# Kernel tuning notes

Measured on AMD Instinct MI355X. Metric: run time of the kernel, lower is better.

The kernel has to match this reference:

```python
import jax, jax.numpy as jnp
import numpy as np

N_NODES = 50000
TAU = 1.0 + (1.0 / 1000.0) * (0.1 - 1.0)  # anneal step 1 -> 0.9991


def setup_inputs() -> dict:
    key = jax.random.key(0)
    ks = jax.random.split(key, 8)
    N, F, H, E, K = N_NODES, 128, 128, 800000, 5
    node_features = jax.random.normal(ks[0], (N, F), dtype=jnp.float32)
    src = jnp.sort(jax.random.randint(ks[1], (E,), 0, N, dtype=jnp.int32))
    dst = jax.random.randint(ks[2], (E,), 0, N, dtype=jnp.int32)
    u_noise = jax.random.uniform(ks[3], (K, E), dtype=jnp.float32,
                                 minval=1e-6, maxval=1.0 - 1e-6)
    # MLP params: Linear(2F -> H), ReLU, Linear(H -> 1)
    W1 = jax.random.normal(ks[4], (2 * F, H), dtype=jnp.float32) / np.sqrt(2 * F)
    b1 = jnp.zeros((H,), dtype=jnp.float32)
    W2 = jax.random.normal(ks[5], (H, 1), dtype=jnp.float32) / np.sqrt(H)
    b2 = jnp.zeros((1,), dtype=jnp.float32)
    return {"node_features": node_features, "W1": W1, "b1": b1,
            "W2": W2, "b2": b2, "u_noise": u_noise, "src": src, "dst": dst}


def reference(node_features, W1, b1, W2, b2, u_noise, src, dst):
    N = N_NODES
    F = node_features.shape[1]
    # per-edge MLP on concat([x_u, x_v]) without materializing the (E, 2F) concat
    x_u = node_features[src]                      # (E, F)
    x_v = node_features[dst]                      # (E, F)
    h = jax.nn.relu(x_u @ W1[:F] + x_v @ W1[F:] + b1)   # (E, H)
    z = (h @ W2 + b2)[:, 0]                       # (E,)
    # per-node (segment) log-softmax over each node's neighbor edges
    zmax = jax.ops.segment_max(z, src, num_segments=N)
    ze = z - zmax[src]
    denom = jax.ops.segment_sum(jnp.exp(ze), src, num_segments=N)
    log_pi = ze - jnp.log(denom)[src]             # (E,)
    # k rounds of Gumbel-softmax sampling
    g = -jnp.log(-jnp.log(u_noise))               # (K, E)
    scores = (log_pi[None, :] + g) / TAU          # (K, E)

    def seg_softmax(s):
        m = jax.ops.segment_max(s, src, num_segments=N)
        e = jnp.exp(s - m[src])
        return e / jax.ops.segment_sum(e, src, num_segments=N)[src]

    def seg_argmax_dst(s):
        m = jax.ops.segment_max(s, src, num_segments=N)
        hit = s >= m[src]
        sel = jax.ops.segment_max(jnp.where(hit, dst, -1), src, num_segments=N)
        return sel  # (N,) selected neighbor per node, per round

    soft = jax.vmap(seg_softmax)(scores)          # (K, E) gumbel-softmax probs
    selected = jax.vmap(seg_argmax_dst)(scores)   # (K, N) sampled neighbor ids
    return selected, soft
```

## Files before the change

### kernel.cpp

```cpp
#include <hip/hip_runtime.h>

#define FEAT 128
#define HID  128
#define XS_S 132

__global__ __launch_bounds__(256) void gemm_ab(
    const float* __restrict__ X, const float* __restrict__ W1,
    float* __restrict__ A, float* __restrict__ B, int N) {
  __shared__ float xs[32 * XS_S];
  __shared__ float ws[32 * 64];
  const int t = threadIdx.x;
  const int n0 = blockIdx.x * 128;
  const int j0 = blockIdx.y * 64;
  const float* Wbase = W1 + (j0 < 128 ? j0 : 128 * HID + (j0 - 128));
  float* Obase = (j0 < 128) ? (A + j0) : (B + (j0 - 128));

  const int tn = t & 31;
  const int tc = t >> 5;

  float acc[4][8];
#pragma unroll
  for (int r = 0; r < 4; ++r)
#pragma unroll
    for (int c = 0; c < 8; ++c) acc[r][c] = 0.f;

  const int ln = t >> 3;
  const int lf = (t & 7) * 4;

  for (int kc = 0; kc < 4; ++kc) {
    __syncthreads();
#pragma unroll
    for (int rep = 0; rep < 4; ++rep) {
      const int nl = ln + rep * 32;
      const int n = n0 + nl;
      float4 v = make_float4(0.f, 0.f, 0.f, 0.f);
      if (n < N) v = *(const float4*)(X + (size_t)n * FEAT + kc * 32 + lf);
      xs[(lf + 0) * XS_S + nl] = v.x;
      xs[(lf + 1) * XS_S + nl] = v.y;
      xs[(lf + 2) * XS_S + nl] = v.z;
      xs[(lf + 3) * XS_S + nl] = v.w;
    }
#pragma unroll
    for (int rep = 0; rep < 2; ++rep) {
      const int idx = rep * 256 + t;
      const int r = idx >> 4;
      const int c4 = (idx & 15) * 4;
      *(float4*)&ws[r * 64 + c4] =
          *(const float4*)(Wbase + (size_t)(kc * 32 + r) * HID + c4);
    }
    __syncthreads();

#pragma unroll 8
    for (int k = 0; k < 32; ++k) {
      const float4 xv = *(const float4*)&xs[k * XS_S + tn * 4];
      const float4 w0 = *(const float4*)&ws[k * 64 + tc * 8];
      const float4 w1 = *(const float4*)&ws[k * 64 + tc * 8 + 4];
      const float xr[4] = {xv.x, xv.y, xv.z, xv.w};
#pragma unroll
      for (int r = 0; r < 4; ++r) {
        acc[r][0] = fmaf(xr[r], w0.x, acc[r][0]);
        acc[r][1] = fmaf(xr[r], w0.y, acc[r][1]);
        acc[r][2] = fmaf(xr[r], w0.z, acc[r][2]);
        acc[r][3] = fmaf(xr[r], w0.w, acc[r][3]);
        acc[r][4] = fmaf(xr[r], w1.x, acc[r][4]);
        acc[r][5] = fmaf(xr[r], w1.y, acc[r][5]);
        acc[r][6] = fmaf(xr[r], w1.z, acc[r][6]);
        acc[r][7] = fmaf(xr[r], w1.w, acc[r][7]);
      }
    }
  }

#pragma unroll
  for (int r = 0; r < 4; ++r) {
    const int n = n0 + tn * 4 + r;
    if (n < N) {
      float* o = Obase + (size_t)n * HID + tc * 8;
      *(float4*)o = make_float4(acc[r][0], acc[r][1], acc[r][2], acc[r][3]);
      *(float4*)(o + 4) = make_float4(acc[r][4], acc[r][5], acc[r][6], acc[r][7]);
    }
  }
}

__global__ __launch_bounds__(256) void row_offsets(
    const int* __restrict__ src, int* __restrict__ rs, int N, int E) {
  const int n = blockIdx.x * 256 + threadIdx.x;
  if (n > N) return;
  int lo = 0, hi = E;
  while (lo < hi) {
    const int mid = (lo + hi) >> 1;
    if (src[mid] < n) lo = mid + 1; else hi = mid;
  }
  rs[n] = lo;
}

__global__ __launch_bounds__(256) void edge_z(
    const float* __restrict__ A, const float* __restrict__ B,
    const float* __restrict__ b1, const float* __restrict__ W2,
    const float* __restrict__ b2, const int* __restrict__ src,
    const int* __restrict__ dst, float* __restrict__ z, int E) {
  const int g = threadIdx.x >> 4;
  const int l = threadIdx.x & 15;
  const int e0 = blockIdx.x * 32 + g * 2;
  if (e0 >= E) return;
  const int e1 = e0 + 1;
  const bool has1 = e1 < E;

  const int u0 = src[e0], v0 = dst[e0];
  const int u1 = has1 ? src[e1] : u0;
  const int v1 = has1 ? dst[e1] : v0;

  const float4* Au0 = (const float4*)(A + (size_t)u0 * HID) + l * 2;
  const float4* Bv0 = (const float4*)(B + (size_t)v0 * HID) + l * 2;
  const float4* Au1 = (const float4*)(A + (size_t)u1 * HID) + l * 2;
  const float4* Bv1 = (const float4*)(B + (size_t)v1 * HID) + l * 2;

  const float4 a00 = Au0[0], a01 = Au0[1];
  const float4 b00 = Bv0[0], b01 = Bv0[1];
  const float4 a10 = Au1[0], a11 = Au1[1];
  const float4 b10 = Bv1[0], b11 = Bv1[1];

  const float4 c0 = *(const float4*)(b1 + l * 8);
  const float4 c1 = *(const float4*)(b1 + l * 8 + 4);
  const float4 w0 = *(const float4*)(W2 + l * 8);
  const float4 w1 = *(const float4*)(W2 + l * 8 + 4);
  const float bias2 = b2[0];

  float p0 = fmaxf(a00.x + b00.x + c0.x, 0.f) * w0.x
           + fmaxf(a00.y + b00.y + c0.y, 0.f) * w0.y
           + fmaxf(a00.z + b00.z + c0.z, 0.f) * w0.z
           + fmaxf(a00.w + b00.w + c0.w, 0.f) * w0.w
           + fmaxf(a01.x + b01.x + c1.x, 0.f) * w1.x
           + fmaxf(a01.y + b01.y + c1.y, 0.f) * w1.y
           + fmaxf(a01.z + b01.z + c1.z, 0.f) * w1.z
           + fmaxf(a01.w + b01.w + c1.w, 0.f) * w1.w;
  float p1 = fmaxf(a10.x + b10.x + c0.x, 0.f) * w0.x
           + fmaxf(a10.y + b10.y + c0.y, 0.f) * w0.y
           + fmaxf(a10.z + b10.z + c0.z, 0.f) * w0.z
           + fmaxf(a10.w + b10.w + c0.w, 0.f) * w0.w
           + fmaxf(a11.x + b11.x + c1.x, 0.f) * w1.x
           + fmaxf(a11.y + b11.y + c1.y, 0.f) * w1.y
           + fmaxf(a11.z + b11.z + c1.z, 0.f) * w1.z
           + fmaxf(a11.w + b11.w + c1.w, 0.f) * w1.w;

#pragma unroll
  for (int m = 8; m >= 1; m >>= 1) {
    p0 += __shfl_xor(p0, m);
    p1 += __shfl_xor(p1, m);
  }
  if (l == 0) {
    z[e0] = p0 + bias2;
    if (has1) z[e1] = p1 + bias2;
  }
}

__global__ __launch_bounds__(256) void seg_sample(
    const float* __restrict__ z, const float* __restrict__ U,
    const int* __restrict__ dst, const int* __restrict__ rs,
    float* __restrict__ out_sel, float* __restrict__ out_soft,
    int N, int E, int K) {
  const int t = threadIdx.x;
  const int lane = t & 63;
  const int half = lane >> 5;
  const int hl = lane & 31;
  const int n = blockIdx.x * 8 + (t >> 6) * 2 + half;
  const float INVTAU = 1.0f / 0.9991f;

  int start = 0, deg = 0;
  if (n < N) { start = rs[n]; deg = rs[n + 1] - start; }

  if (__all(deg <= 32)) {
    if (n >= N) return;
    if (deg == 0) {
      if (hl == 0)
        for (int k = 0; k < K; ++k) out_sel[(size_t)k * N + n] = -2147483648.0f;
      return;
    }
    const bool act = hl < deg;
    const int e = start + (act ? hl : 0);
    const float zv = act ? z[e] : -INFINITY;
    const int d = act ? dst[e] : -1;

    float zmax = zv;
#pragma unroll
    for (int m = 16; m >= 1; m >>= 1) zmax = fmaxf(zmax, __shfl_xor(zmax, m));
    float den = act ? __expf(zv - zmax) : 0.f;
#pragma unroll
    for (int m = 16; m >= 1; m >>= 1) den += __shfl_xor(den, m);
    const float lpb = (zv - zmax) - __logf(den);

    for (int k = 0; k < K; ++k) {
      float ex = 0.f;
      if (act) {
        const float uu = U[(size_t)k * E + e];
        const float t2 = -__logf(uu);
        const float g = -__logf(t2);
        ex = __expf((lpb + g) * INVTAU);
      }
      float d2 = ex;
      float mx = ex;
      int md = d;
#pragma unroll
      for (int m = 16; m >= 1; m >>= 1) {
        d2 += __shfl_xor(d2, m);
        const float ox = __shfl_xor(mx, m);
        const int od = __shfl_xor(md, m);
        if (ox > mx) { mx = ox; md = od; }
        else if (ox == mx) md = max(md, od);
      }
      if (hl == 0) out_sel[(size_t)k * N + n] = (float)md;
      if (act) {
        const float inv = __builtin_amdgcn_rcpf(d2);
        out_soft[(size_t)k * E + e] = ex * inv;
      }
    }
    return;
  }

  const int wbase = blockIdx.x * 8 + (t >> 6) * 2;
  for (int j = 0; j < 2; ++j) {
    const int nn = wbase + j;
    if (nn >= N) continue;
    const int st = rs[nn];
    const int dg = rs[nn + 1] - st;
    if (dg == 0) {
      if (lane == 0)
        for (int k = 0; k < K; ++k) out_sel[(size_t)k * N + nn] = -2147483648.0f;
      continue;
    }
    float zmax = -INFINITY;
    for (int c = lane; c < dg; c += 64) zmax = fmaxf(zmax, z[st + c]);
#pragma unroll
    for (int m = 32; m >= 1; m >>= 1) zmax = fmaxf(zmax, __shfl_xor(zmax, m));
    float den = 0.f;
    for (int c = lane; c < dg; c += 64) den += expf(z[st + c] - zmax);
#pragma unroll
    for (int m = 32; m >= 1; m >>= 1) den += __shfl_xor(den, m);
    const float logd = logf(den);

    for (int k = 0; k < K; ++k) {
      float m2 = -INFINITY;
      for (int c = lane; c < dg; c += 64) {
        const int e = st + c;
        const float g = -logf(-logf(U[(size_t)k * E + e]));
        const float s = ((z[e] - zmax) - logd + g) * INVTAU;
        m2 = fmaxf(m2, s);
      }
#pragma unroll
      for (int m = 32; m >= 1; m >>= 1) m2 = fmaxf(m2, __shfl_xor(m2, m));
      float d2 = 0.f;
      int cand = -1;
      for (int c = lane; c < dg; c += 64) {
        const int e = st + c;
        const float g = -logf(-logf(U[(size_t)k * E + e]));
        const float s = ((z[e] - zmax) - logd + g) * INVTAU;
        d2 += expf(s - m2);
        if (s >= m2) cand = max(cand, dst[e]);
      }
#pragma unroll
      for (int m = 32; m >= 1; m >>= 1) d2 += __shfl_xor(d2, m);
#pragma unroll
      for (int m = 32; m >= 1; m >>= 1) cand = max(cand, __shfl_xor(cand, m));
      if (lane == 0) out_sel[(size_t)k * N + nn] = (float)cand;
      for (int c = lane; c < dg; c += 64) {
        const int e = st + c;
        const float g = -logf(-logf(U[(size_t)k * E + e]));
        const float s = ((z[e] - zmax) - logd + g) * INVTAU;
        out_soft[(size_t)k * E + e] = expf(s - m2) / d2;
      }
    }
  }
}

extern "C" void kernel_launch(void* const* d_in, const int* in_sizes, int n_in,
                              void* d_out, int out_size, void* d_ws, size_t ws_size,
                              hipStream_t stream) {
  const float* X  = (const float*)d_in[0];
  const float* W1 = (const float*)d_in[1];
  const float* b1 = (const float*)d_in[2];
  const float* W2 = (const float*)d_in[3];
  const float* b2 = (const float*)d_in[4];
  const float* U  = (const float*)d_in[5];
  const int* src  = (const int*)d_in[6];
  const int* dst  = (const int*)d_in[7];
  const int E = in_sizes[6];
  const int K = in_sizes[5] / E;
  const int N = in_sizes[0] / FEAT;

  float* A = (float*)d_ws;
  float* B = A + (size_t)N * HID;
  float* z = B + (size_t)N * HID;
  int* rs  = (int*)(z + E);

  float* out_sel  = (float*)d_out;
  float* out_soft = (float*)d_out + (size_t)K * N;

  hipLaunchKernelGGL(gemm_ab, dim3((N + 127) / 128, 4), dim3(256), 0, stream,
                     X, W1, A, B, N);
  hipLaunchKernelGGL(row_offsets, dim3((N + 256) / 256), dim3(256), 0, stream,
                     src, rs, N, E);
  hipLaunchKernelGGL(edge_z, dim3((E + 31) / 32), dim3(256), 0, stream,
                     A, B, b1, W2, b2, src, dst, z, E);
  hipLaunchKernelGGL(seg_sample, dim3((N + 7) / 8), dim3(256), 0, stream,
                     z, U, dst, rs, out_sel, out_soft, N, E, K);
}
```

Measured before the change: 241.4 us.

## Widen GEMM tile with XCD-aware block mapping, fold b1, 16-lane segment sampling

The node GEMM now computes all 128 output columns per block, so each thread holds a 4x16 accumulator instead of 4x8 and the X tile is loaded half as often. A 1D grid is remapped so neighbouring node tiles land on the same XCD. The b1 bias is added once per node in the GEMM epilogue rather than per edge in edge_z. seg_sample now assigns 16 lanes per node, each handling two edges, which cuts shuffle steps and packs more nodes per wave but makes the __all(deg<=32) fast path slower for high-degree nodes and raises GEMM register pressure.

```diff
diff --git a/kernel.cpp b/kernel.cpp
--- a/kernel.cpp
+++ b/kernel.cpp
@@ -6,23 +6,29 @@
 
 __global__ __launch_bounds__(256) void gemm_ab(
     const float* __restrict__ X, const float* __restrict__ W1,
-    float* __restrict__ A, float* __restrict__ B, int N) {
+    const float* __restrict__ b1, float* __restrict__ A,
+    float* __restrict__ B, int N) {
   __shared__ float xs[32 * XS_S];
-  __shared__ float ws[32 * 64];
+  __shared__ float ws[32 * 128];
   const int t = threadIdx.x;
-  const int n0 = blockIdx.x * 128;
-  const int j0 = blockIdx.y * 64;
-  const float* Wbase = W1 + (j0 < 128 ? j0 : 128 * HID + (j0 - 128));
-  float* Obase = (j0 < 128) ? (A + j0) : (B + (j0 - 128));
+
+  const int nb = gridDim.x;
+  const int q = nb >> 3, r = nb & 7;
+  const int xcd = blockIdx.x & 7, bidx = blockIdx.x >> 3;
+  const int nw = (xcd < r ? xcd * (q + 1) : r * (q + 1) + (xcd - r) * q) + bidx;
+  const int n0 = (nw >> 1) * 128;
+  const int g = nw & 1;
+  const float* Wbase = W1 + (size_t)g * 128 * HID;
+  float* Obase = g ? B : A;
 
   const int tn = t & 31;
   const int tc = t >> 5;
 
-  float acc[4][8];
-#pragma unroll
-  for (int r = 0; r < 4; ++r)
-#pragma unroll
-    for (int c = 0; c < 8; ++c) acc[r][c] = 0.f;
+  float acc[4][16];
+#pragma unroll
+  for (int rr = 0; rr < 4; ++rr)
+#pragma unroll
+    for (int c = 0; c < 16; ++c) acc[rr][c] = 0.f;
 
   const int ln = t >> 3;
   const int lf = (t & 7) * 4;
@@ -41,42 +47,63 @@
       xs[(lf + 3) * XS_S + nl] = v.w;
     }
 #pragma unroll
-    for (int rep = 0; rep < 2; ++rep) {
+    for (int rep = 0; rep < 4; ++rep) {
       const int idx = rep * 256 + t;
-      const int r = idx >> 4;
-      const int c4 = (idx & 15) * 4;
-      *(float4*)&ws[r * 64 + c4] =
-          *(const float4*)(Wbase + (size_t)(kc * 32 + r) * HID + c4);
+      const int wr = idx >> 5;
+      const int c4 = (idx & 31) * 4;
+      *(float4*)&ws[wr * 128 + c4] =
+          *(const float4*)(Wbase + (size_t)(kc * 32 + wr) * HID + c4);
     }
     __syncthreads();
 
 #pragma unroll 8
     for (int k = 0; k < 32; ++k) {
       const float4 xv = *(const float4*)&xs[k * XS_S + tn * 4];
-      const float4 w0 = *(const float4*)&ws[k * 64 + tc * 8];
-      const float4 w1 = *(const float4*)&ws[k * 64 + tc * 8 + 4];
+      const float4 w0 = *(const float4*)&ws[k * 128 + tc * 16 + 0];
+      const float4 w1 = *(const float4*)&ws[k * 128 + tc * 16 + 4];
+      const float4 w2 = *(const float4*)&ws[k * 128 + tc * 16 + 8];
+      const float4 w3 = *(const float4*)&ws[k * 128 + tc * 16 + 12];
       const float xr[4] = {xv.x, xv.y, xv.z, xv.w};
 #pragma unroll
-      for (int r = 0; r < 4; ++r) {
-        acc[r][0] = fmaf(xr[r], w0.x, acc[r][0]);
-        acc[r][1] = fmaf(xr[r], w0.y, acc[r][1]);
-        acc[r][2] = fmaf(xr[r], w0.z, acc[r][2]);
-        acc[r][3] = fmaf(xr[r], w0.w, acc[r][3]);
-        acc[r][4] = fmaf(xr[r], w1.x, acc[r][4]);
-        acc[r][5] = fmaf(xr[r], w1.y, acc[r][5]);
-        acc[r][6] = fmaf(xr[r], w1.z, acc[r][6]);
-        acc[r][7] = fmaf(xr[r], w1.w, acc[r][7]);
-      }
-    }
-  }
-
-#pragma unroll
-  for (int r = 0; r < 4; ++r) {
-    const int n = n0 + tn * 4 + r;
+      for (int rr = 0; rr < 4; ++rr) {
+        acc[rr][0]  = fmaf(xr[rr], w0.x, acc[rr][0]);
+        acc[rr][1]  = fmaf(xr[rr], w0.y, acc[rr][1]);
+        acc[rr][2]  = fmaf(xr[rr], w0.z, acc[rr][2]);
+        acc[rr][3]  = fmaf(xr[rr], w0.w, acc[rr][3]);
+        acc[rr][4]  = fmaf(xr[rr], w1.x, acc[rr][4]);
+        acc[rr][5]  = fmaf(xr[rr], w1.y, acc[rr][5]);
+        acc[rr][6]  = fmaf(xr[rr], w1.z, acc[rr][6]);
+        acc[rr][7]  = fmaf(xr[rr], w1.w, acc[rr][7]);
+        acc[rr][8]  = fmaf(xr[rr], w2.x, acc[rr][8]);
+        acc[rr][9]  = fmaf(xr[rr], w2.y, acc[rr][9]);
+        acc[rr][10] = fmaf(xr[rr], w2.z, acc[rr][10]);
+        acc[rr][11] = fmaf(xr[rr], w2.w, acc[rr][11]);
+        acc[rr][12] = fmaf(xr[rr], w3.x, acc[rr][12]);
+        acc[rr][13] = fmaf(xr[rr], w3.y, acc[rr][13]);
+        acc[rr][14] = fmaf(xr[rr], w3.z, acc[rr][14]);
+        acc[rr][15] = fmaf(xr[rr], w3.w, acc[rr][15]);
+      }
+    }
+  }
+
+  float4 bb[4];
+#pragma unroll
+  for (int c = 0; c < 4; ++c) bb[c] = make_float4(0.f, 0.f, 0.f, 0.f);
+  if (g == 0) {
+#pragma unroll
+    for (int c = 0; c < 4; ++c) bb[c] = *(const float4*)(b1 + tc * 16 + c * 4);
+  }
+#pragma unroll
+  for (int rr = 0; rr < 4; ++rr) {
+    const int n = n0 + tn * 4 + rr;
     if (n < N) {
-      float* o = Obase + (size_t)n * HID + tc * 8;
-      *(float4*)o = make_float4(acc[r][0], acc[r][1], acc[r][2], acc[r][3]);
-      *(float4*)(o + 4) = make_float4(acc[r][4], acc[r][5], acc[r][6], acc[r][7]);
+      float* o = Obase + (size_t)n * HID + tc * 16;
+#pragma unroll
+      for (int c = 0; c < 4; ++c) {
+        *(float4*)(o + c * 4) = make_float4(
+            acc[rr][c * 4 + 0] + bb[c].x, acc[rr][c * 4 + 1] + bb[c].y,
+            acc[rr][c * 4 + 2] + bb[c].z, acc[rr][c * 4 + 3] + bb[c].w);
+      }
     }
   }
 }
@@ -95,9 +122,9 @@
 
 __global__ __launch_bounds__(256) void edge_z(
     const float* __restrict__ A, const float* __restrict__ B,
-    const float* __restrict__ b1, const float* __restrict__ W2,
-    const float* __restrict__ b2, const int* __restrict__ src,
-    const int* __restrict__ dst, float* __restrict__ z, int E) {
+    const float* __restrict__ W2, const float* __restrict__ b2,
+    const int* __restrict__ src, const int* __restrict__ dst,
+    float* __restrict__ z, int E) {
   const int g = threadIdx.x >> 4;
   const int l = threadIdx.x & 15;
   const int e0 = blockIdx.x * 32 + g * 2;
@@ -119,28 +146,26 @@
   const float4 a10 = Au1[0], a11 = Au1[1];
   const float4 b10 = Bv1[0], b11 = Bv1[1];
 
-  const float4 c0 = *(const float4*)(b1 + l * 8);
-  const float4 c1 = *(const float4*)(b1 + l * 8 + 4);
   const float4 w0 = *(const float4*)(W2 + l * 8);
   const float4 w1 = *(const float4*)(W2 + l * 8 + 4);
   const float bias2 = b2[0];
 
-  float p0 = fmaxf(a00.x + b00.x + c0.x, 0.f) * w0.x
-           + fmaxf(a00.y + b00.y + c0.y, 0.f) * w0.y
-           + fmaxf(a00.z + b00.z + c0.z, 0.f) * w0.z
-           + fmaxf(a00.w + b00.w + c0.w, 0.f) * w0.w
-           + fmaxf(a01.x + b01.x + c1.x, 0.f) * w1.x
-           + fmaxf(a01.y + b01.y + c1.y, 0.f) * w1.y
-           + fmaxf(a01.z + b01.z + c1.z, 0.f) * w1.z
-           + fmaxf(a01.w + b01.w + c1.w, 0.f) * w1.w;
-  float p1 = fmaxf(a10.x + b10.x + c0.x, 0.f) * w0.x
-           + fmaxf(a10.y + b10.y + c0.y, 0.f) * w0.y
-           + fmaxf(a10.z + b10.z + c0.z, 0.f) * w0.z
-           + fmaxf(a10.w + b10.w + c0.w, 0.f) * w0.w
-           + fmaxf(a11.x + b11.x + c1.x, 0.f) * w1.x
-           + fmaxf(a11.y + b11.y + c1.y, 0.f) * w1.y
-           + fmaxf(a11.z + b11.z + c1.z, 0.f) * w1.z
-           + fmaxf(a11.w + b11.w + c1.w, 0.f) * w1.w;
+  float p0 = fmaxf(a00.x + b00.x, 0.f) * w0.x
+           + fmaxf(a00.y + b00.y, 0.f) * w0.y
+           + fmaxf(a00.z + b00.z, 0.f) * w0.z
+           + fmaxf(a00.w + b00.w, 0.f) * w0.w
+           + fmaxf(a01.x + b01.x, 0.f) * w1.x
+           + fmaxf(a01.y + b01.y, 0.f) * w1.y
+           + fmaxf(a01.z + b01.z, 0.f) * w1.z
+           + fmaxf(a01.w + b01.w, 0.f) * w1.w;
+  float p1 = fmaxf(a10.x + b10.x, 0.f) * w0.x
+           + fmaxf(a10.y + b10.y, 0.f) * w0.y
+           + fmaxf(a10.z + b10.z, 0.f) * w0.z
+           + fmaxf(a10.w + b10.w, 0.f) * w0.w
+           + fmaxf(a11.x + b11.x, 0.f) * w1.x
+           + fmaxf(a11.y + b11.y, 0.f) * w1.y
+           + fmaxf(a11.z + b11.z, 0.f) * w1.z
+           + fmaxf(a11.w + b11.w, 0.f) * w1.w;
 
 #pragma unroll
   for (int m = 8; m >= 1; m >>= 1) {
@@ -160,9 +185,9 @@
     int N, int E, int K) {
   const int t = threadIdx.x;
   const int lane = t & 63;
-  const int half = lane >> 5;
-  const int hl = lane & 31;
-  const int n = blockIdx.x * 8 + (t >> 6) * 2 + half;
+  const int qtr = lane >> 4;
+  const int ql = lane & 15;
+  const int n = blockIdx.x * 16 + (t >> 6) * 4 + qtr;
   const float INVTAU = 1.0f / 0.9991f;
 
   int start = 0, deg = 0;
@@ -171,53 +196,65 @@
   if (__all(deg <= 32)) {
     if (n >= N) return;
     if (deg == 0) {
-      if (hl == 0)
+      if (ql == 0)
         for (int k = 0; k < K; ++k) out_sel[(size_t)k * N + n] = -2147483648.0f;
       return;
     }
-    const bool act = hl < deg;
-    const int e = start + (act ? hl : 0);
-    const float zv = act ? z[e] : -INFINITY;
-    const int d = act ? dst[e] : -1;
-
-    float zmax = zv;
-#pragma unroll
-    for (int m = 16; m >= 1; m >>= 1) zmax = fmaxf(zmax, __shfl_xor(zmax, m));
-    float den = act ? __expf(zv - zmax) : 0.f;
-#pragma unroll
-    for (int m = 16; m >= 1; m >>= 1) den += __shfl_xor(den, m);
-    const float lpb = (zv - zmax) - __logf(den);
+    const bool a0 = 2 * ql < deg;
+    const bool a1 = 2 * ql + 1 < deg;
+    const int e0 = start + 2 * ql;
+    const int e1 = e0 + 1;
+    const float z0 = a0 ? z[e0] : -INFINITY;
+    const float z1 = a1 ? z[e1] : -INFINITY;
+    const int d0 = a0 ? dst[e0] : -1;
+    const int d1 = a1 ? dst[e1] : -1;
+
+    float zmax = fmaxf(z0, z1);
+#pragma unroll
+    for (int m = 8; m >= 1; m >>= 1) zmax = fmaxf(zmax, __shfl_xor(zmax, m));
+    float den = (a0 ? __expf(z0 - zmax) : 0.f) + (a1 ? __expf(z1 - zmax) : 0.f);
+#pragma unroll
+    for (int m = 8; m >= 1; m >>= 1) den += __shfl_xor(den, m);
+    const float logd = __logf(den);
+    const float lp0 = (z0 - zmax) - logd;
+    const float lp1 = (z1 - zmax) - logd;
 
     for (int k = 0; k < K; ++k) {
-      float ex = 0.f;
-      if (act) {
-        const float uu = U[(size_t)k * E + e];
-        const float t2 = -__logf(uu);
-        const float g = -__logf(t2);
-        ex = __expf((lpb + g) * INVTAU);
-      }
-      float d2 = ex;
-      float mx = ex;
-      int md = d;
-#pragma unroll
-      for (int m = 16; m >= 1; m >>= 1) {
+      float ex0 = 0.f, ex1 = 0.f;
+      if (a0) {
+        const float uu = U[(size_t)k * E + e0];
+        const float gum = -__logf(-__logf(uu));
+        ex0 = __expf((lp0 + gum) * INVTAU);
+      }
+      if (a1) {
+        const float uu = U[(size_t)k * E + e1];
+        const float gum = -__logf(-__logf(uu));
+        ex1 = __expf((lp1 + gum) * INVTAU);
+      }
+      float d2 = ex0 + ex1;
+      float mx;
+      int md;
+      if (ex1 > ex0)      { mx = ex1; md = d1; }
+      else if (ex1 < ex0) { mx = ex0; md = d0; }
+      else                { mx = ex0; md = max(d0, d1); }
+#pragma unroll
+      for (int m = 8; m >= 1; m >>= 1) {
         d2 += __shfl_xor(d2, m);
         const float ox = __shfl_xor(mx, m);
         const int od = __shfl_xor(md, m);
         if (ox > mx) { mx = ox; md = od; }
         else if (ox == mx) md = max(md, od);
       }
-      if (hl == 0) out_sel[(size_t)k * N + n] = (float)md;
-      if (act) {
-        const float inv = __builtin_amdgcn_rcpf(d2);
-        out_soft[(size_t)k * E + e] = ex * inv;
-      }
+      if (ql == 0) out_sel[(size_t)k * N + n] = (float)md;
+      const float inv = __builtin_amdgcn_rcpf(d2);
+      if (a0) out_soft[(size_t)k * E + e0] = ex0 * inv;
+      if (a1) out_soft[(size_t)k * E + e1] = ex1 * inv;
     }
     return;
   }
 
-  const int wbase = blockIdx.x * 8 + (t >> 6) * 2;
-  for (int j = 0; j < 2; ++j) {
+  const int wbase = blockIdx.x * 16 + (t >> 6) * 4;
+  for (int j = 0; j < 4; ++j) {
     const int nn = wbase + j;
     if (nn >= N) continue;
     const int st = rs[nn];
@@ -241,8 +278,8 @@
       float m2 = -INFINITY;
       for (int c = lane; c < dg; c += 64) {
         const int e = st + c;
-        const float g = -logf(-logf(U[(size_t)k * E + e]));
-        const float s = ((z[e] - zmax) - logd + g) * INVTAU;
+        const float gum = -logf(-logf(U[(size_t)k * E + e]));
+        const float s = ((z[e] - zmax) - logd + gum) * INVTAU;
         m2 = fmaxf(m2, s);
       }
 #pragma unroll
@@ -251,8 +288,8 @@
       int cand = -1;
       for (int c = lane; c < dg; c += 64) {
         const int e = st + c;
-        const float g = -logf(-logf(U[(size_t)k * E + e]));
-        const float s = ((z[e] - zmax) - logd + g) * INVTAU;
+        const float gum = -logf(-logf(U[(size_t)k * E + e]));
+        const float s = ((z[e] - zmax) - logd + gum) * INVTAU;
         d2 += expf(s - m2);
         if (s >= m2) cand = max(cand, dst[e]);
       }
@@ -263,8 +300,8 @@
       if (lane == 0) out_sel[(size_t)k * N + nn] = (float)cand;
       for (int c = lane; c < dg; c += 64) {
         const int e = st + c;
-        const float g = -logf(-logf(U[(size_t)k * E + e]));
-        const float s = ((z[e] - zmax) - logd + g) * INVTAU;
+        const float gum = -logf(-logf(U[(size_t)k * E + e]));
+        const float s = ((z[e] - zmax) - logd + gum) * INVTAU;
         out_soft[(size_t)k * E + e] = expf(s - m2) / d2;
       }
     }
@@ -294,12 +331,12 @@
   float* out_sel  = (float*)d_out;
   float* out_soft = (float*)d_out + (size_t)K * N;
 
-  hipLaunchKernelGGL(gemm_ab, dim3((N + 127) / 128, 4), dim3(256), 0, stream,
-                     X, W1, A, B, N);
+  hipLaunchKernelGGL(gemm_ab, dim3(2 * ((N + 127) / 128)), dim3(256), 0, stream,
+                     X, W1, b1, A, B, N);
   hipLaunchKernelGGL(row_offsets, dim3((N + 256) / 256), dim3(256), 0, stream,
                      src, rs, N, E);
   hipLaunchKernelGGL(edge_z, dim3((E + 31) / 32), dim3(256), 0, stream,
-                     A, B, b1, W2, b2, src, dst, z, E);
-  hipLaunchKernelGGL(seg_sample, dim3((N + 7) / 8), dim3(256), 0, stream,
+                     A, B, W2, b2, src, dst, z, E);
+  hipLaunchKernelGGL(seg_sample, dim3((N + 15) / 16), dim3(256), 0, stream,
                      z, U, dst, rs, out_sel, out_soft, N, E, K);
 }
```

Result: no change. 246.0 us (+1.9%).
